# Performance work log

Measured on AMD Instinct MI355X. Metric: run time of the kernel, lower is better.

## Reference

```python
import jax, jax.numpy as jnp
import numpy as np
from jax import lax

B, N, C = 32, 2048, 256
S, NSAMP, RADIUS = 128, 16, 0.3
NH, NS, NC = 12, 10, 10
OUT_DIM = 5 + 2 * NH + 4 * NS + NC  # 79
EPS = 1e-5
MEAN_SIZES = np.array([[0.76584, 1.398258, 0.472728], [2.114256, 1.6203, 0.927272], [0.404671, 1.071108, 1.688889], [0.591958, 0.552978, 0.827272], [0.69519, 1.346299, 0.736364], [0.528526, 1.002642, 1.172878], [0.500618, 0.632163, 0.683424], [0.923508, 1.867419, 0.845495], [0.791118, 1.279516, 0.718182], [0.699104, 0.454178, 0.75625]], dtype=np.float32)


def _bn(x, g, be, m, v):
    # eval-mode batchnorm over trailing channel dim
    return (x - m) * (g / jnp.sqrt(v + EPS)) + be


def _fps(xyz, npoint):
    # farthest point sampling, sequential over npoint via scan, vectorized over batch
    Bb, Nn, _ = xyz.shape
    def step(carry, _):
        mind, last = carry  # [B,N], [B]
        lp = jnp.take_along_axis(xyz, last[:, None, None], axis=1)  # [B,1,3]
        d = jnp.sum((xyz - lp) ** 2, axis=-1)
        mind = jnp.minimum(mind, d)
        nxt = jnp.argmax(mind, axis=-1).astype(jnp.int32)
        return (mind, nxt), last
    init = (jnp.full((Bb, Nn), 1e10, xyz.dtype), jnp.zeros((Bb,), jnp.int32))
    _, inds = lax.scan(step, init, None, length=npoint)
    return jnp.transpose(inds)  # [B, npoint]


def _ball_query(xyz, new_xyz, radius, nsample):
    # first-nsample points within radius of each center (pad with first hit)
    Nn = xyz.shape[1]
    d2 = jnp.sum((new_xyz[:, :, None, :] - xyz[:, None, :, :]) ** 2, axis=-1)  # [B,S,N]
    cand = jnp.where(d2 < radius * radius, jnp.arange(Nn, dtype=jnp.int32)[None, None, :], Nn)
    idx = jnp.sort(cand, axis=-1)[..., :nsample]
    first = idx[..., :1]  # center itself is always within radius (d=0)
    return jnp.where(idx == Nn, first, idx)


def _forward(xyz, features, w0, bb0, g0, be0, m0, v0, w1, bb1, g1, be1, m1, v1, w2, bb2, g2, be2, m2, v2, c1w, c1b, g3, be3, m3, v3, c2w, c2b, g4, be4, m4, v4, c3w, c3b):
    fps_idx = _fps(xyz, S)  # [B,S]
    new_xyz = jnp.take_along_axis(xyz, fps_idx[..., None], axis=1)  # [B,S,3]
    idx = _ball_query(xyz, new_xyz, RADIUS, NSAMP)  # [B,S,ns]
    bidx = jnp.arange(xyz.shape[0])[:, None, None]
    g_xyz = (xyz[bidx, idx] - new_xyz[:, :, None, :]) / RADIUS  # normalize_xyz
    g_feat = jnp.transpose(features, (0, 2, 1))[bidx, idx]  # [B,S,ns,C]
    x = jnp.concatenate([g_xyz, g_feat], axis=-1)  # [B,S,ns,C+3]
    for w, bb, g, be, m, v in ((w0, bb0, g0, be0, m0, v0), (w1, bb1, g1, be1, m1, v1), (w2, bb2, g2, be2, m2, v2)):
        x = jax.nn.relu(_bn(x @ w + bb, g, be, m, v))
    x = jnp.max(x, axis=2)  # [B,S,128] pooled features
    net = jax.nn.relu(_bn(x @ c1w + c1b, g3, be3, m3, v3))
    net = jax.nn.relu(_bn(net @ c2w + c2b, g4, be4, m4, v4))
    net = net @ c3w + c3b  # [B,S,79] == torch net.transpose(2,1)
    obj = net[..., 0:2]
    ctr = new_xyz + net[..., 2:5]
    hs = net[..., 5:5 + NH]
    hrn = net[..., 5 + NH:5 + 2 * NH]
    hr = hrn * jnp.float32(np.pi / NH)
    ss = net[..., 5 + 2 * NH:5 + 2 * NH + NS]
    srn = net[..., 5 + 2 * NH + NS:5 + 2 * NH + 4 * NS].reshape(net.shape[0], S, NS, 3)
    sr = srn * jnp.asarray(MEAN_SIZES)[None, None]
    sem = net[..., 5 + 2 * NH + 4 * NS:]
    return jnp.concatenate([new_xyz, obj, ctr, hs, hrn, hr, ss, srn.reshape(net.shape[0], S, NS * 3), sr.reshape(net.shape[0], S, NS * 3), sem], axis=-1)  # [B,S,124]


def setup_inputs() -> dict:
    key = jax.random.key(0)
    ks = jax.random.split(key, 40)
    def w(k, shp):
        return jax.random.normal(k, shp, jnp.float32) * 0.05
    d = {"xyz": jax.random.normal(ks[0], (B, N, 3), jnp.float32), "features": jax.random.normal(ks[1], (B, C, N), jnp.float32)}
    i = 2
    for li, (cin, cout) in enumerate(((C + 3, 128), (128, 128), (128, 128))):
        d[f"w{li}"] = w(ks[i], (cin, cout)); d[f"bb{li}"] = w(ks[i + 1], (cout,))
        d[f"g{li}"] = 1.0 + w(ks[i + 2], (cout,)); d[f"be{li}"] = w(ks[i + 3], (cout,))
        d[f"m{li}"] = w(ks[i + 4], (cout,)); d[f"v{li}"] = jnp.ones((cout,), jnp.float32)
        i += 5
    d["c1w"] = w(ks[i], (128, 128)); d["c1b"] = w(ks[i + 1], (128,))
    d["g3"] = 1.0 + w(ks[i + 2], (128,)); d["be3"] = w(ks[i + 3], (128,)); d["m3"] = w(ks[i + 4], (128,)); d["v3"] = jnp.ones((128,), jnp.float32)
    d["c2w"] = w(ks[i + 5], (128, 128)); d["c2b"] = w(ks[i + 6], (128,))
    d["g4"] = 1.0 + w(ks[i + 7], (128,)); d["be4"] = w(ks[i + 8], (128,)); d["m4"] = w(ks[i + 9], (128,)); d["v4"] = jnp.ones((128,), jnp.float32)
    d["c3w"] = w(ks[i + 10], (128, OUT_DIM)); d["c3b"] = w(ks[i + 11], (OUT_DIM,))
    return d


def reference(xyz, features, w0, bb0, g0, be0, m0, v0, w1, bb1, g1, be1, m1, v1, w2, bb2, g2, be2, m2, v2, c1w, c1b, g3, be3, m3, v3, c2w, c2b, g4, be4, m4, v4, c3w, c3b):
    return _forward(xyz, features, w0, bb0, g0, be0, m0, v0, w1, bb1, g1, be1, m1, v1, w2, bb2, g2, be2, m2, v2, c1w, c1b, g3, be3, m3, v3, c2w, c2b, g4, be4, m4, v4, c3w, c3b)
```

## Files before the change

kernel.cpp:

```cpp
#include <hip/hip_runtime.h>
#include <hip/hip_bf16.h>
#include <math.h>

#define Bn 32
#define Nn 2048
#define Cc 256
#define Sn 128
#define KK 16
#define H 128
#define OUTC 79
#define ODIM 124
#define KP1 288

typedef __attribute__((ext_vector_type(8))) short short8;
typedef __attribute__((ext_vector_type(4))) float f32x4;
typedef unsigned long long ull;

__device__ __constant__ float MEANF[30] = {
    0.76584f, 1.398258f, 0.472728f,
    2.114256f, 1.6203f, 0.927272f,
    0.404671f, 1.071108f, 1.688889f,
    0.591958f, 0.552978f, 0.827272f,
    0.69519f, 1.346299f, 0.736364f,
    0.528526f, 1.002642f, 1.172878f,
    0.500618f, 0.632163f, 0.683424f,
    0.923508f, 1.867419f, 0.845495f,
    0.791118f, 1.279516f, 0.718182f,
    0.699104f, 0.454178f, 0.75625f};

__device__ __forceinline__ unsigned short f2bf(float f) {
    __hip_bfloat16 h = __float2bfloat16(f);
    return *reinterpret_cast<unsigned short*>(&h);
}

__device__ __forceinline__ ull umax64(ull a, ull b) { return a > b ? a : b; }

#define DPPMAX(CTRL, RM)                                                        \
    {                                                                           \
        const int nhi = __builtin_amdgcn_update_dpp(0, hi, CTRL, RM, 0xf, false); \
        const int nlo = __builtin_amdgcn_update_dpp(0, lo, CTRL, RM, 0xf, false); \
        const ull nk = ((ull)(unsigned)nhi << 32) | (unsigned)nlo;              \
        const ull ck = ((ull)(unsigned)hi << 32) | (unsigned)lo;                \
        if (nk > ck) { hi = nhi; lo = nlo; }                                    \
    }

struct SmemFPS {
    float xs[Nn * 3];
    ull red[2][4];
    float nx[Sn * 3];
};
struct SmemT {
    float tile[64][33];
};
__global__ __launch_bounds__(256) void fps_transpose_kernel(const float* __restrict__ xyz,
                                                            const float* __restrict__ features,
                                                            float* __restrict__ new_xyz,
                                                            unsigned short* __restrict__ fT) {
    __shared__ __align__(16) char smem_raw[sizeof(SmemT) > sizeof(SmemFPS) ? sizeof(SmemT)
                                                                           : sizeof(SmemFPS)];
    const int bid = blockIdx.x;
    if (bid >= Bn) {
        SmemT* sm = (SmemT*)smem_raw;
        const int tb = bid - Bn;
        const int b = tb >> 8;
        const int rem = tb & 255;
        const int n0 = (rem & 63) * 32;
        const int c0 = (rem >> 6) * 64;
        const int tx = threadIdx.x & 31;
        const int ty = threadIdx.x >> 5;
        for (int i = ty; i < 64; i += 8)
            sm->tile[i][tx] = features[((size_t)b * Cc + (c0 + i)) * Nn + n0 + tx];
        __syncthreads();
        for (int n = ty; n < 32; n += 8) {
            const float lo = sm->tile[tx * 2 + 0][n];
            const float hi = sm->tile[tx * 2 + 1][n];
            const unsigned int v = (unsigned int)f2bf(lo) | ((unsigned int)f2bf(hi) << 16);
            *reinterpret_cast<unsigned int*>(&fT[((size_t)b * Nn + (n0 + n)) * Cc + c0 + tx * 2]) = v;
        }
        return;
    }
    {
#pragma clang fp contract(off)
        SmemFPS* sm = (SmemFPS*)smem_raw;
        float* xs = sm->xs;
        const int b = bid;
        const int t = threadIdx.x;
        const int lane = t & 63;
        const int wv = t >> 6;

        {
            float4* xs4 = (float4*)xs;
            const float4* src = (const float4*)(xyz + (size_t)b * Nn * 3);
            for (int i = t; i < Nn * 3 / 4; i += 256) xs4[i] = src[i];
        }
        __syncthreads();

        const int base = wv * 512 + lane;
        float px[8], py[8], pz[8], mind[8];
        int klo[8];
#pragma unroll
        for (int j = 0; j < 8; j++) {
            const int p = base + j * 64;
            px[j] = xs[p * 3 + 0];
            py[j] = xs[p * 3 + 1];
            pz[j] = xs[p * 3 + 2];
            mind[j] = 1e10f;
            klo[j] = 2047 - p;
        }
        float lx = xs[0], ly = xs[1], lz = xs[2];

        for (int it = 0; it < Sn; ++it) {
            if (t == 0) {
                sm->nx[it * 3 + 0] = lx;
                sm->nx[it * 3 + 1] = ly;
                sm->nx[it * 3 + 2] = lz;
            }
            ull kk[8];
#pragma unroll
            for (int j = 0; j < 8; j++) {
                const float dx = px[j] - lx;
                const float dy = py[j] - ly;
                const float dz = pz[j] - lz;
                const float dx2 = dx * dx;
                const float dy2 = dy * dy;
                const float dz2 = dz * dz;
                const float s01 = dx2 + dy2;
                const float d = s01 + dz2;
                const float m = fminf(mind[j], d);
                mind[j] = m;
                kk[j] = ((ull)__float_as_uint(m) << 32) | (unsigned int)klo[j];
            }
            ull k0 = umax64(kk[0], kk[1]);
            ull k1 = umax64(kk[2], kk[3]);
            ull k2 = umax64(kk[4], kk[5]);
            ull k3 = umax64(kk[6], kk[7]);
            k0 = umax64(k0, k1);
            k2 = umax64(k2, k3);
            const ull bk0 = umax64(k0, k2);

            int hi = (int)(bk0 >> 32);
            int lo = (int)(bk0 & 0xffffffffull);
            DPPMAX(0x111, 0xf)
            DPPMAX(0x112, 0xf)
            DPPMAX(0x114, 0xf)
            DPPMAX(0x118, 0xf)
            DPPMAX(0x142, 0xa)
            DPPMAX(0x143, 0xc)

            if (lane == 63)
                sm->red[it & 1][wv] = ((ull)(unsigned)hi << 32) | (unsigned)lo;
            __syncthreads();
            ull r0 = sm->red[it & 1][0];
            ull r1 = sm->red[it & 1][1];
            ull r2 = sm->red[it & 1][2];
            ull r3 = sm->red[it & 1][3];
            const ull bk = umax64(umax64(r0, r1), umax64(r2, r3));
            const int last = 2047 - (int)(bk & 0xffffffffull);
            lx = xs[last * 3 + 0];
            ly = xs[last * 3 + 1];
            lz = xs[last * 3 + 2];
        }
        __syncthreads();
        for (int i = t; i < Sn * 3; i += 256)
            new_xyz[(size_t)b * Sn * 3 + i] = sm->nx[i];
    }
}

__device__ __forceinline__ float w0val(const float* __restrict__ w0, int n, int k) {
    if (k < 256) return w0[(3 + k) * H + n];
    if (k < 259) return w0[(k - 256) * H + n];
    return 0.0f;
}

__global__ __launch_bounds__(256) void prep_kernel(
    const float* __restrict__ w0, const float* __restrict__ bb0,
    const float* __restrict__ g0, const float* __restrict__ be0,
    const float* __restrict__ m0, const float* __restrict__ v0,
    const float* __restrict__ w1, const float* __restrict__ bb1,
    const float* __restrict__ g1, const float* __restrict__ be1,
    const float* __restrict__ m1, const float* __restrict__ v1,
    const float* __restrict__ w2, const float* __restrict__ bb2,
    const float* __restrict__ g2, const float* __restrict__ be2,
    const float* __restrict__ m2, const float* __restrict__ v2,
    const float* __restrict__ c1w, const float* __restrict__ c1b,
    const float* __restrict__ g3, const float* __restrict__ be3,
    const float* __restrict__ m3, const float* __restrict__ v3,
    const float* __restrict__ c2w, const float* __restrict__ c2b,
    const float* __restrict__ g4, const float* __restrict__ be4,
    const float* __restrict__ m4, const float* __restrict__ v4,
    const float* __restrict__ c3w, const float* __restrict__ c3b,
    unsigned short* __restrict__ Wf0, unsigned short* __restrict__ Wf1,
    unsigned short* __restrict__ Wf2, unsigned short* __restrict__ Wfc1,
    unsigned short* __restrict__ Wfc2, unsigned short* __restrict__ Wfc3,
    float* __restrict__ scbi, float* __restrict__ scbiH) {
    const int idx = blockIdx.x * 256 + threadIdx.x;

    if (idx < 4608) {
        const int kc = idx / 512;
        const int rem = idx & 511;
        const int nt = rem >> 6;
        const int lane = rem & 63;
        const int n = nt * 16 + (lane & 15);
        const int kb = kc * 32 + (lane >> 4) * 8;
        union { unsigned short u[8]; uint4 q; } P;
#pragma unroll
        for (int j = 0; j < 8; j++) P.u[j] = f2bf(w0val(w0, n, kb + j));
        ((uint4*)Wf0)[idx] = P.q;
    }
    if (idx < 2048) {
        const int kc = idx >> 9;
        const int rem = idx & 511;
        const int nt = rem >> 6;
        const int lane = rem & 63;
        const int n = nt * 16 + (lane & 15);
        const int kb = kc * 32 + (lane >> 4) * 8;
        union { unsigned short u[8]; uint4 q; } P1, P2, P3, P4;
#pragma unroll
        for (int j = 0; j < 8; j++) {
            const int k = kb + j;
            P1.u[j] = f2bf(w1[k * H + n]);
            P2.u[j] = f2bf(w2[k * H + n]);
            P3.u[j] = f2bf(c1w[k * H + n]);
            P4.u[j] = f2bf(c2w[k * H + n]);
        }
        ((uint4*)Wf1)[idx] = P1.q;
        ((uint4*)Wf2)[idx] = P2.q;
        ((uint4*)Wfc1)[idx] = P3.q;
        ((uint4*)Wfc2)[idx] = P4.q;
    }
    if (idx < 1280) {
        const int kc = idx / 320;
        const int rem = idx % 320;
        const int nt = rem / 64;
        const int lane = rem % 64;
        const int n = nt * 16 + (lane & 15);
        const int kb = kc * 32 + (lane >> 4) * 8;
        union { unsigned short u[8]; uint4 q; } P;
#pragma unroll
        for (int j = 0; j < 8; j++)
            P.u[j] = (n < OUTC) ? f2bf(c3w[(kb + j) * OUTC + n]) : (unsigned short)0;
        ((uint4*)Wfc3)[idx] = P.q;
    }
    if (idx < 128) {
        const float sc1 = g0[idx] / sqrtf(v0[idx] + 1e-5f);
        scbi[0 * 128 + idx] = sc1;
        scbi[1 * 128 + idx] = (bb0[idx] - m0[idx]) * sc1 + be0[idx];
        const float sc2 = g1[idx] / sqrtf(v1[idx] + 1e-5f);
        scbi[2 * 128 + idx] = sc2;
        scbi[3 * 128 + idx] = (bb1[idx] - m1[idx]) * sc2 + be1[idx];
        const float sc3 = g2[idx] / sqrtf(v2[idx] + 1e-5f);
        scbi[4 * 128 + idx] = sc3;
        scbi[5 * 128 + idx] = (bb2[idx] - m2[idx]) * sc3 + be2[idx];
        const float sA = g3[idx] / sqrtf(v3[idx] + 1e-5f);
        scbiH[0 * 128 + idx] = sA;
        scbiH[1 * 128 + idx] = (c1b[idx] - m3[idx]) * sA + be3[idx];
        const float sB = g4[idx] / sqrtf(v4[idx] + 1e-5f);
        scbiH[2 * 128 + idx] = sB;
        scbiH[3 * 128 + idx] = (c2b[idx] - m4[idx]) * sB + be4[idx];
    }
    if (idx < 80) scbiH[512 + idx] = (idx < OUTC) ? c3b[idx] : 0.0f;
}

#define YSTR 136
__global__ __launch_bounds__(256) void groupmlp_mfma_kernel(
    const float* __restrict__ xyz, const unsigned short* __restrict__ featT,
    const float* __restrict__ new_xyz,
    const unsigned short* __restrict__ Wf0, const unsigned short* __restrict__ Wf1,
    const unsigned short* __restrict__ Wf2, const float* __restrict__ scbi,
    unsigned short* __restrict__ pooledb) {
    const int wv = threadIdx.x >> 6;
    const int lane = threadIdx.x & 63;
    const int bs = blockIdx.x * 4 + wv;
    const int b = bs >> 7;
    const int mrow = lane & 15;
    const int quad = lane >> 4;

    __shared__ unsigned short ylds_all[4][16 * YSTR];
    __shared__ int sbuf[4][16];
    unsigned short* ylds = &ylds_all[wv][0];

    const float cx = new_xyz[bs * 3 + 0];
    const float cy = new_xyz[bs * 3 + 1];
    const float cz = new_xyz[bs * 3 + 2];
    int basec = 0;
    {
#pragma clang fp contract(off)
        for (int c0 = 0; c0 < Nn && basec < KK; c0 += 64) {
            const int p = c0 + lane;
            const float dx = xyz[((size_t)b * Nn + p) * 3 + 0] - cx;
            const float dy = xyz[((size_t)b * Nn + p) * 3 + 1] - cy;
            const float dz = xyz[((size_t)b * Nn + p) * 3 + 2] - cz;
            const float dx2 = dx * dx;
            const float dy2 = dy * dy;
            const float dz2 = dz * dz;
            const float s01 = dx2 + dy2;
            const float d2 = s01 + dz2;
            const bool q = d2 < 0.09f;
            const ull mask = __ballot(q);
            const int prefix = __popcll(mask & ((1ull << lane) - 1ull));
            const int slot = basec + prefix;
            if (q && slot < KK) sbuf[wv][slot] = p;
            basec += __popcll(mask);
        }
    }
    const int cnt = basec < KK ? basec : KK;
    const int p = sbuf[wv][mrow < cnt ? mrow : 0];

    const short8* arow = reinterpret_cast<const short8*>(featT + ((size_t)(b * Nn + p)) * Cc);

    short8 a1x = {0, 0, 0, 0, 0, 0, 0, 0};
    {
        const float fx = xyz[((size_t)(b * Nn + p)) * 3 + 0];
        const float fy = xyz[((size_t)(b * Nn + p)) * 3 + 1];
        const float fz = xyz[((size_t)(b * Nn + p)) * 3 + 2];
        if (quad == 0) {
            a1x.s0 = (short)f2bf((fx - cx) / 0.3f);
            a1x.s1 = (short)f2bf((fy - cy) / 0.3f);
            a1x.s2 = (short)f2bf((fz - cz) / 0.3f);
        }
    }

    const short8* wf0 = reinterpret_cast<const short8*>(Wf0);
    const short8* wf1 = reinterpret_cast<const short8*>(Wf1);
    const short8* wf2 = reinterpret_cast<const short8*>(Wf2);
    const short8* yv = reinterpret_cast<const short8*>(ylds);

    f32x4 acc[8] = {};

    {
        short8 acur = arow[quad];
        short8 anxt;
        short8 bcur[8], bnxt[8];
#pragma unroll
        for (int nt = 0; nt < 8; nt++)
            bcur[nt] = wf0[nt * 64 + lane];
        for (int kc = 0; kc < 9; kc++) {
            if (kc < 8) {
                if (kc < 7) anxt = arow[(kc + 1) * 4 + quad];
                else anxt = a1x;
#pragma unroll
                for (int nt = 0; nt < 8; nt++)
                    bnxt[nt] = wf0[((kc + 1) * 8 + nt) * 64 + lane];
            }
#pragma unroll
            for (int nt = 0; nt < 8; nt++)
                acc[nt] = __builtin_amdgcn_mfma_f32_16x16x32_bf16(acur, bcur[nt], acc[nt], 0, 0, 0);
            acur = anxt;
#pragma unroll
            for (int nt = 0; nt < 8; nt++) bcur[nt] = bnxt[nt];
        }
    }
#pragma unroll
    for (int nt = 0; nt < 8; nt++) {
        const int n = nt * 16 + mrow;
        const float sc = scbi[0 * 128 + n];
        const float bi = scbi[1 * 128 + n];
#pragma unroll
        for (int r = 0; r < 4; r++) {
            const float z = fmaxf(acc[nt][r] * sc + bi, 0.0f);
            ylds[(quad * 4 + r) * YSTR + n] = f2bf(z);
        }
    }

#pragma unroll
    for (int nt = 0; nt < 8; nt++) acc[nt] = (f32x4){0.f, 0.f, 0.f, 0.f};
    {
        short8 acur = yv[mrow * (YSTR / 8) + quad];
        short8 anxt;
        short8 bcur[8], bnxt[8];
#pragma unroll
        for (int nt = 0; nt < 8; nt++)
            bcur[nt] = wf1[nt * 64 + lane];
        for (int kc = 0; kc < 4; kc++) {
            if (kc < 3) {
                anxt = yv[mrow * (YSTR / 8) + (kc + 1) * 4 + quad];
#pragma unroll
                for (int nt = 0; nt < 8; nt++)
                    bnxt[nt] = wf1[((kc + 1) * 8 + nt) * 64 + lane];
            }
#pragma unroll
            for (int nt = 0; nt < 8; nt++)
                acc[nt] = __builtin_amdgcn_mfma_f32_16x16x32_bf16(acur, bcur[nt], acc[nt], 0, 0, 0);
            acur = anxt;
#pragma unroll
            for (int nt = 0; nt < 8; nt++) bcur[nt] = bnxt[nt];
        }
    }
#pragma unroll
    for (int nt = 0; nt < 8; nt++) {
        const int n = nt * 16 + mrow;
        const float sc = scbi[2 * 128 + n];
        const float bi = scbi[3 * 128 + n];
#pragma unroll
        for (int r = 0; r < 4; r++) {
            const float z = fmaxf(acc[nt][r] * sc + bi, 0.0f);
            ylds[(quad * 4 + r) * YSTR + n] = f2bf(z);
        }
    }

#pragma unroll
    for (int nt = 0; nt < 8; nt++) acc[nt] = (f32x4){0.f, 0.f, 0.f, 0.f};
    {
        short8 acur = yv[mrow * (YSTR / 8) + quad];
        short8 anxt;
        short8 bcur[8], bnxt[8];
#pragma unroll
        for (int nt = 0; nt < 8; nt++)
            bcur[nt] = wf2[nt * 64 + lane];
        for (int kc = 0; kc < 4; kc++) {
            if (kc < 3) {
                anxt = yv[mrow * (YSTR / 8) + (kc + 1) * 4 + quad];
#pragma unroll
                for (int nt = 0; nt < 8; nt++)
                    bnxt[nt] = wf2[((kc + 1) * 8 + nt) * 64 + lane];
            }
#pragma unroll
            for (int nt = 0; nt < 8; nt++)
                acc[nt] = __builtin_amdgcn_mfma_f32_16x16x32_bf16(acur, bcur[nt], acc[nt], 0, 0, 0);
            acur = anxt;
#pragma unroll
            for (int nt = 0; nt < 8; nt++) bcur[nt] = bnxt[nt];
        }
    }
#pragma unroll
    for (int nt = 0; nt < 8; nt++) {
        const int n = nt * 16 + mrow;
        const float sc = scbi[4 * 128 + n];
        const float bi = scbi[5 * 128 + n];
        float vmax = 0.0f;
#pragma unroll
        for (int r = 0; r < 4; r++)
            vmax = fmaxf(vmax, acc[nt][r] * sc + bi);
        vmax = fmaxf(vmax, __shfl_xor(vmax, 16));
        vmax = fmaxf(vmax, __shfl_xor(vmax, 32));
        if (quad == 0) pooledb[(size_t)bs * H + n] = f2bf(vmax);
    }
}

__global__ __launch_bounds__(64) void head_mfma_kernel(
    const unsigned short* __restrict__ pooledb, const float* __restrict__ new_xyz,
    const unsigned short* __restrict__ Wfc1, const unsigned short* __restrict__ Wfc2,
    const unsigned short* __restrict__ Wfc3, const float* __restrict__ scbiH,
    float* __restrict__ out) {
    const int lane = threadIdx.x;
    const int row0 = blockIdx.x * 16;
    const int mrow = lane & 15;
    const int quad = lane >> 4;

    __shared__ unsigned short ylds[16 * YSTR];
    __shared__ float flds[16 * 84];

    const short8* ar = reinterpret_cast<const short8*>(pooledb + (size_t)(row0 + mrow) * H);
    const short8* w1h = reinterpret_cast<const short8*>(Wfc1);
    const short8* w2h = reinterpret_cast<const short8*>(Wfc2);
    const short8* w3h = reinterpret_cast<const short8*>(Wfc3);
    const short8* yv = reinterpret_cast<const short8*>(ylds);

    f32x4 acc[8] = {};
#pragma unroll
    for (int kc = 0; kc < 4; kc++) {
        const short8 a = ar[kc * 4 + quad];
#pragma unroll
        for (int nt = 0; nt < 8; nt++) {
            const short8 bf = w1h[(kc * 8 + nt) * 64 + lane];
            acc[nt] = __builtin_amdgcn_mfma_f32_16x16x32_bf16(a, bf, acc[nt], 0, 0, 0);
        }
    }
#pragma unroll
    for (int nt = 0; nt < 8; nt++) {
        const int n = nt * 16 + mrow;
        const float sc = scbiH[0 * 128 + n];
        const float bi = scbiH[1 * 128 + n];
#pragma unroll
        for (int r = 0; r < 4; r++) {
            const float z = fmaxf(acc[nt][r] * sc + bi, 0.0f);
            ylds[(quad * 4 + r) * YSTR + n] = f2bf(z);
        }
    }

#pragma unroll
    for (int nt = 0; nt < 8; nt++) acc[nt] = (f32x4){0.f, 0.f, 0.f, 0.f};
#pragma unroll
    for (int kc = 0; kc < 4; kc++) {
        const short8 a = yv[mrow * (YSTR / 8) + kc * 4 + quad];
#pragma unroll
        for (int nt = 0; nt < 8; nt++) {
            const short8 bf = w2h[(kc * 8 + nt) * 64 + lane];
            acc[nt] = __builtin_amdgcn_mfma_f32_16x16x32_bf16(a, bf, acc[nt], 0, 0, 0);
        }
    }
#pragma unroll
    for (int nt = 0; nt < 8; nt++) {
        const int n = nt * 16 + mrow;
        const float sc = scbiH[2 * 128 + n];
        const float bi = scbiH[3 * 128 + n];
#pragma unroll
        for (int r = 0; r < 4; r++) {
            const float z = fmaxf(acc[nt][r] * sc + bi, 0.0f);
            ylds[(quad * 4 + r) * YSTR + n] = f2bf(z);
        }
    }

    f32x4 acc3[5] = {};
#pragma unroll
    for (int kc = 0; kc < 4; kc++) {
        const short8 a = yv[mrow * (YSTR / 8) + kc * 4 + quad];
#pragma unroll
        for (int nt = 0; nt < 5; nt++) {
            const short8 bf = w3h[(kc * 5 + nt) * 64 + lane];
            acc3[nt] = __builtin_amdgcn_mfma_f32_16x16x32_bf16(a, bf, acc3[nt], 0, 0, 0);
        }
    }
#pragma unroll
    for (int nt = 0; nt < 5; nt++) {
        const int n = nt * 16 + mrow;
        const float bi = scbiH[512 + n];
#pragma unroll
        for (int r = 0; r < 4; r++)
            flds[(quad * 4 + r) * 84 + n] = acc3[nt][r] + bi;
    }

    for (int m = 0; m < 16; m++) {
        const int row = row0 + m;
        const float* net = &flds[m * 84];
        const float* nz = new_xyz + (size_t)row * 3;
#pragma unroll
        for (int jj = 0; jj < 2; jj++) {
            const int j = lane + jj * 64;
            if (j < ODIM) {
                float val;
                if (j < 3) val = nz[j];
                else if (j < 5) val = net[j - 3];
                else if (j < 8) val = nz[j - 5] + net[2 + (j - 5)];
                else if (j < 20) val = net[5 + (j - 8)];
                else if (j < 32) val = net[17 + (j - 20)];
                else if (j < 44) val = net[17 + (j - 32)] * (float)(3.14159265358979323846 / 12.0);
                else if (j < 54) val = net[29 + (j - 44)];
                else if (j < 84) val = net[39 + (j - 54)];
                else if (j < 114) val = net[39 + (j - 84)] * MEANF[j - 84];
                else val = net[69 + (j - 114)];
                out[(size_t)row * ODIM + j] = val;
            }
        }
    }
}

extern "C" void kernel_launch(void* const* d_in, const int* in_sizes, int n_in,
                              void* d_out, int out_size, void* d_ws, size_t ws_size,
                              hipStream_t stream) {
    (void)in_sizes; (void)n_in; (void)out_size; (void)ws_size;
    const float* xyz = (const float*)d_in[0];
    const float* features = (const float*)d_in[1];
    const float* w0 = (const float*)d_in[2];
    const float* bb0 = (const float*)d_in[3];
    const float* g0 = (const float*)d_in[4];
    const float* be0 = (const float*)d_in[5];
    const float* m0 = (const float*)d_in[6];
    const float* v0 = (const float*)d_in[7];
    const float* w1 = (const float*)d_in[8];
    const float* bb1 = (const float*)d_in[9];
    const float* g1 = (const float*)d_in[10];
    const float* be1 = (const float*)d_in[11];
    const float* m1 = (const float*)d_in[12];
    const float* v1 = (const float*)d_in[13];
    const float* w2 = (const float*)d_in[14];
    const float* bb2 = (const float*)d_in[15];
    const float* g2 = (const float*)d_in[16];
    const float* be2 = (const float*)d_in[17];
    const float* m2 = (const float*)d_in[18];
    const float* v2 = (const float*)d_in[19];
    const float* c1w = (const float*)d_in[20];
    const float* c1b = (const float*)d_in[21];
    const float* g3 = (const float*)d_in[22];
    const float* be3 = (const float*)d_in[23];
    const float* m3 = (const float*)d_in[24];
    const float* v3 = (const float*)d_in[25];
    const float* c2w = (const float*)d_in[26];
    const float* c2b = (const float*)d_in[27];
    const float* g4 = (const float*)d_in[28];
    const float* be4 = (const float*)d_in[29];
    const float* m4 = (const float*)d_in[30];
    const float* v4 = (const float*)d_in[31];
    const float* c3w = (const float*)d_in[32];
    const float* c3b = (const float*)d_in[33];
    float* out = (float*)d_out;

    char* ws = (char*)d_ws;
    float* nxyz = (float*)(ws + 0);
    float* scbi = (float*)(ws + 49152);
    float* scbiH = (float*)(ws + 52224);
    unsigned short* Wf0 = (unsigned short*)(ws + 54592);
    unsigned short* Wf1 = (unsigned short*)(ws + 128320);
    unsigned short* Wf2 = (unsigned short*)(ws + 161088);
    unsigned short* Wfc1 = (unsigned short*)(ws + 193856);
    unsigned short* Wfc2 = (unsigned short*)(ws + 226624);
    unsigned short* Wfc3 = (unsigned short*)(ws + 259392);
    unsigned short* pooledb = (unsigned short*)(ws + 279872);
    unsigned short* featT = (unsigned short*)(ws + 804160);

    hipLaunchKernelGGL(prep_kernel, dim3(18), dim3(256), 0, stream,
                       w0, bb0, g0, be0, m0, v0,
                       w1, bb1, g1, be1, m1, v1,
                       w2, bb2, g2, be2, m2, v2,
                       c1w, c1b, g3, be3, m3, v3,
                       c2w, c2b, g4, be4, m4, v4,
                       c3w, c3b,
                       Wf0, Wf1, Wf2, Wfc1, Wfc2, Wfc3, scbi, scbiH);
    hipLaunchKernelGGL(fps_transpose_kernel, dim3(Bn + Bn * 256), dim3(256), 0, stream,
                       xyz, features, nxyz, featT);
    hipLaunchKernelGGL(groupmlp_mfma_kernel, dim3(Bn * Sn / 4), dim3(256), 0, stream,
                       xyz, featT, nxyz, Wf0, Wf1, Wf2, scbi, pooledb);
    hipLaunchKernelGGL(head_mfma_kernel, dim3(Bn * Sn / 16), dim3(64), 0, stream,
                       pooledb, nxyz, Wfc1, Wfc2, Wfc3, scbiH, out);
}
```

Baseline: 279.9 us.

## Merge prep into front kernel and fuse group MLP with head MLP

Weight preparation now runs as extra blocks of the FPS/transpose kernel, which cuts the launch count from four to two. The grouped MLP and the head MLP are fused into one tail kernel. Each 256-thread block now handles 16 centers: pooled features stay in LDS as bf16, and the head GEMMs are split across four waves with block barriers between stages. This removes the pooled-feature round trip through global memory and two launch gaps, at the cost of fewer, larger tail blocks (256 instead of 1024 blocks) and extra synchronisation.

```diff
diff --git a/kernel.cpp b/kernel.cpp
--- a/kernel.cpp
+++ b/kernel.cpp
@@ -11,6 +11,7 @@
 #define OUTC 79
 #define ODIM 124
 #define KP1 288
+#define YSTR 136
 
 typedef __attribute__((ext_vector_type(8))) short short8;
 typedef __attribute__((ext_vector_type(4))) float f32x4;
@@ -35,13 +36,19 @@
 
 __device__ __forceinline__ ull umax64(ull a, ull b) { return a > b ? a : b; }
 
-#define DPPMAX(CTRL, RM)                                                        \
-    {                                                                           \
+__device__ __forceinline__ float w0val(const float* __restrict__ w0, int n, int k) {
+    if (k < 256) return w0[(3 + k) * H + n];
+    if (k < 259) return w0[(k - 256) * H + n];
+    return 0.0f;
+}
+
+#define DPPMAX(CTRL, RM)                                                          \
+    {                                                                             \
         const int nhi = __builtin_amdgcn_update_dpp(0, hi, CTRL, RM, 0xf, false); \
         const int nlo = __builtin_amdgcn_update_dpp(0, lo, CTRL, RM, 0xf, false); \
-        const ull nk = ((ull)(unsigned)nhi << 32) | (unsigned)nlo;              \
-        const ull ck = ((ull)(unsigned)hi << 32) | (unsigned)lo;                \
-        if (nk > ck) { hi = nhi; lo = nlo; }                                    \
+        const ull nk = ((ull)(unsigned)nhi << 32) | (unsigned)nlo;                \
+        const ull ck = ((ull)(unsigned)hi << 32) | (unsigned)lo;                  \
+        if (nk > ck) { hi = nhi; lo = nlo; }                                      \
     }
 
 struct SmemFPS {
@@ -52,127 +59,9 @@
 struct SmemT {
     float tile[64][33];
 };
-__global__ __launch_bounds__(256) void fps_transpose_kernel(const float* __restrict__ xyz,
-                                                            const float* __restrict__ features,
-                                                            float* __restrict__ new_xyz,
-                                                            unsigned short* __restrict__ fT) {
-    __shared__ __align__(16) char smem_raw[sizeof(SmemT) > sizeof(SmemFPS) ? sizeof(SmemT)
-                                                                           : sizeof(SmemFPS)];
-    const int bid = blockIdx.x;
-    if (bid >= Bn) {
-        SmemT* sm = (SmemT*)smem_raw;
-        const int tb = bid - Bn;
-        const int b = tb >> 8;
-        const int rem = tb & 255;
-        const int n0 = (rem & 63) * 32;
-        const int c0 = (rem >> 6) * 64;
-        const int tx = threadIdx.x & 31;
-        const int ty = threadIdx.x >> 5;
-        for (int i = ty; i < 64; i += 8)
-            sm->tile[i][tx] = features[((size_t)b * Cc + (c0 + i)) * Nn + n0 + tx];
-        __syncthreads();
-        for (int n = ty; n < 32; n += 8) {
-            const float lo = sm->tile[tx * 2 + 0][n];
-            const float hi = sm->tile[tx * 2 + 1][n];
-            const unsigned int v = (unsigned int)f2bf(lo) | ((unsigned int)f2bf(hi) << 16);
-            *reinterpret_cast<unsigned int*>(&fT[((size_t)b * Nn + (n0 + n)) * Cc + c0 + tx * 2]) = v;
-        }
-        return;
-    }
-    {
-#pragma clang fp contract(off)
-        SmemFPS* sm = (SmemFPS*)smem_raw;
-        float* xs = sm->xs;
-        const int b = bid;
-        const int t = threadIdx.x;
-        const int lane = t & 63;
-        const int wv = t >> 6;
-
-        {
-            float4* xs4 = (float4*)xs;
-            const float4* src = (const float4*)(xyz + (size_t)b * Nn * 3);
-            for (int i = t; i < Nn * 3 / 4; i += 256) xs4[i] = src[i];
-        }
-        __syncthreads();
-
-        const int base = wv * 512 + lane;
-        float px[8], py[8], pz[8], mind[8];
-        int klo[8];
-#pragma unroll
-        for (int j = 0; j < 8; j++) {
-            const int p = base + j * 64;
-            px[j] = xs[p * 3 + 0];
-            py[j] = xs[p * 3 + 1];
-            pz[j] = xs[p * 3 + 2];
-            mind[j] = 1e10f;
-            klo[j] = 2047 - p;
-        }
-        float lx = xs[0], ly = xs[1], lz = xs[2];
-
-        for (int it = 0; it < Sn; ++it) {
-            if (t == 0) {
-                sm->nx[it * 3 + 0] = lx;
-                sm->nx[it * 3 + 1] = ly;
-                sm->nx[it * 3 + 2] = lz;
-            }
-            ull kk[8];
-#pragma unroll
-            for (int j = 0; j < 8; j++) {
-                const float dx = px[j] - lx;
-                const float dy = py[j] - ly;
-                const float dz = pz[j] - lz;
-                const float dx2 = dx * dx;
-                const float dy2 = dy * dy;
-                const float dz2 = dz * dz;
-                const float s01 = dx2 + dy2;
-                const float d = s01 + dz2;
-                const float m = fminf(mind[j], d);
-                mind[j] = m;
-                kk[j] = ((ull)__float_as_uint(m) << 32) | (unsigned int)klo[j];
-            }
-            ull k0 = umax64(kk[0], kk[1]);
-            ull k1 = umax64(kk[2], kk[3]);
-            ull k2 = umax64(kk[4], kk[5]);
-            ull k3 = umax64(kk[6], kk[7]);
-            k0 = umax64(k0, k1);
-            k2 = umax64(k2, k3);
-            const ull bk0 = umax64(k0, k2);
-
-            int hi = (int)(bk0 >> 32);
-            int lo = (int)(bk0 & 0xffffffffull);
-            DPPMAX(0x111, 0xf)
-            DPPMAX(0x112, 0xf)
-            DPPMAX(0x114, 0xf)
-            DPPMAX(0x118, 0xf)
-            DPPMAX(0x142, 0xa)
-            DPPMAX(0x143, 0xc)
-
-            if (lane == 63)
-                sm->red[it & 1][wv] = ((ull)(unsigned)hi << 32) | (unsigned)lo;
-            __syncthreads();
-            ull r0 = sm->red[it & 1][0];
-            ull r1 = sm->red[it & 1][1];
-            ull r2 = sm->red[it & 1][2];
-            ull r3 = sm->red[it & 1][3];
-            const ull bk = umax64(umax64(r0, r1), umax64(r2, r3));
-            const int last = 2047 - (int)(bk & 0xffffffffull);
-            lx = xs[last * 3 + 0];
-            ly = xs[last * 3 + 1];
-            lz = xs[last * 3 + 2];
-        }
-        __syncthreads();
-        for (int i = t; i < Sn * 3; i += 256)
-            new_xyz[(size_t)b * Sn * 3 + i] = sm->nx[i];
-    }
-}
-
-__device__ __forceinline__ float w0val(const float* __restrict__ w0, int n, int k) {
-    if (k < 256) return w0[(3 + k) * H + n];
-    if (k < 259) return w0[(k - 256) * H + n];
-    return 0.0f;
-}
-
-__global__ __launch_bounds__(256) void prep_kernel(
+__global__ __launch_bounds__(256) void front_kernel(
+    const float* __restrict__ xyz, const float* __restrict__ features,
+    float* __restrict__ new_xyz, unsigned short* __restrict__ fT,
     const float* __restrict__ w0, const float* __restrict__ bb0,
     const float* __restrict__ g0, const float* __restrict__ be0,
     const float* __restrict__ m0, const float* __restrict__ v0,
@@ -193,334 +82,445 @@
     unsigned short* __restrict__ Wf2, unsigned short* __restrict__ Wfc1,
     unsigned short* __restrict__ Wfc2, unsigned short* __restrict__ Wfc3,
     float* __restrict__ scbi, float* __restrict__ scbiH) {
-    const int idx = blockIdx.x * 256 + threadIdx.x;
-
-    if (idx < 4608) {
-        const int kc = idx / 512;
-        const int rem = idx & 511;
-        const int nt = rem >> 6;
-        const int lane = rem & 63;
-        const int n = nt * 16 + (lane & 15);
-        const int kb = kc * 32 + (lane >> 4) * 8;
-        union { unsigned short u[8]; uint4 q; } P;
-#pragma unroll
-        for (int j = 0; j < 8; j++) P.u[j] = f2bf(w0val(w0, n, kb + j));
-        ((uint4*)Wf0)[idx] = P.q;
-    }
-    if (idx < 2048) {
-        const int kc = idx >> 9;
-        const int rem = idx & 511;
-        const int nt = rem >> 6;
-        const int lane = rem & 63;
-        const int n = nt * 16 + (lane & 15);
-        const int kb = kc * 32 + (lane >> 4) * 8;
-        union { unsigned short u[8]; uint4 q; } P1, P2, P3, P4;
+    __shared__ __align__(16) char smem_raw[sizeof(SmemT) > sizeof(SmemFPS) ? sizeof(SmemT)
+                                                                           : sizeof(SmemFPS)];
+    const int bid = blockIdx.x;
+    if (bid >= Bn + 8192) {
+        const int idx = (bid - (Bn + 8192)) * 256 + threadIdx.x;
+        if (idx < 4608) {
+            const int kc = idx / 512;
+            const int rem = idx & 511;
+            const int nt = rem >> 6;
+            const int ln = rem & 63;
+            const int n = nt * 16 + (ln & 15);
+            const int kb = kc * 32 + (ln >> 4) * 8;
+            union { unsigned short u[8]; uint4 q; } P;
+#pragma unroll
+            for (int j = 0; j < 8; j++) P.u[j] = f2bf(w0val(w0, n, kb + j));
+            ((uint4*)Wf0)[idx] = P.q;
+        }
+        if (idx < 2048) {
+            const int kc = idx >> 9;
+            const int rem = idx & 511;
+            const int nt = rem >> 6;
+            const int ln = rem & 63;
+            const int n = nt * 16 + (ln & 15);
+            const int kb = kc * 32 + (ln >> 4) * 8;
+            union { unsigned short u[8]; uint4 q; } P1, P2, P3, P4;
+#pragma unroll
+            for (int j = 0; j < 8; j++) {
+                const int k = kb + j;
+                P1.u[j] = f2bf(w1[k * H + n]);
+                P2.u[j] = f2bf(w2[k * H + n]);
+                P3.u[j] = f2bf(c1w[k * H + n]);
+                P4.u[j] = f2bf(c2w[k * H + n]);
+            }
+            ((uint4*)Wf1)[idx] = P1.q;
+            ((uint4*)Wf2)[idx] = P2.q;
+            ((uint4*)Wfc1)[idx] = P3.q;
+            ((uint4*)Wfc2)[idx] = P4.q;
+        }
+        if (idx < 1280) {
+            const int kc = idx / 320;
+            const int rem = idx % 320;
+            const int nt = rem / 64;
+            const int ln = rem % 64;
+            const int n = nt * 16 + (ln & 15);
+            const int kb = kc * 32 + (ln >> 4) * 8;
+            union { unsigned short u[8]; uint4 q; } P;
+#pragma unroll
+            for (int j = 0; j < 8; j++)
+                P.u[j] = (n < OUTC) ? f2bf(c3w[(kb + j) * OUTC + n]) : (unsigned short)0;
+            ((uint4*)Wfc3)[idx] = P.q;
+        }
+        if (idx < 128) {
+            const float sc1 = g0[idx] / sqrtf(v0[idx] + 1e-5f);
+            scbi[0 * 128 + idx] = sc1;
+            scbi[1 * 128 + idx] = (bb0[idx] - m0[idx]) * sc1 + be0[idx];
+            const float sc2 = g1[idx] / sqrtf(v1[idx] + 1e-5f);
+            scbi[2 * 128 + idx] = sc2;
+            scbi[3 * 128 + idx] = (bb1[idx] - m1[idx]) * sc2 + be1[idx];
+            const float sc3 = g2[idx] / sqrtf(v2[idx] + 1e-5f);
+            scbi[4 * 128 + idx] = sc3;
+            scbi[5 * 128 + idx] = (bb2[idx] - m2[idx]) * sc3 + be2[idx];
+            const float sA = g3[idx] / sqrtf(v3[idx] + 1e-5f);
+            scbiH[0 * 128 + idx] = sA;
+            scbiH[1 * 128 + idx] = (c1b[idx] - m3[idx]) * sA + be3[idx];
+            const float sB = g4[idx] / sqrtf(v4[idx] + 1e-5f);
+            scbiH[2 * 128 + idx] = sB;
+            scbiH[3 * 128 + idx] = (c2b[idx] - m4[idx]) * sB + be4[idx];
+        }
+        if (idx < 80) scbiH[512 + idx] = (idx < OUTC) ? c3b[idx] : 0.0f;
+        return;
+    }
+    if (bid >= Bn) {
+        SmemT* sm = (SmemT*)smem_raw;
+        const int tb = bid - Bn;
+        const int b = tb >> 8;
+        const int rem = tb & 255;
+        const int n0 = (rem & 63) * 32;
+        const int c0 = (rem >> 6) * 64;
+        const int tx = threadIdx.x & 31;
+        const int ty = threadIdx.x >> 5;
+        for (int i = ty; i < 64; i += 8)
+            sm->tile[i][tx] = features[((size_t)b * Cc + (c0 + i)) * Nn + n0 + tx];
+        __syncthreads();
+        for (int n = ty; n < 32; n += 8) {
+            const float lo2 = sm->tile[tx * 2 + 0][n];
+            const float hi2 = sm->tile[tx * 2 + 1][n];
+            const unsigned int v = (unsigned int)f2bf(lo2) | ((unsigned int)f2bf(hi2) << 16);
+            *reinterpret_cast<unsigned int*>(&fT[((size_t)b * Nn + (n0 + n)) * Cc + c0 + tx * 2]) = v;
+        }
+        return;
+    }
+    {
+#pragma clang fp contract(off)
+        SmemFPS* sm = (SmemFPS*)smem_raw;
+        float* xs = sm->xs;
+        const int b = bid;
+        const int t = threadIdx.x;
+        const int lane = t & 63;
+        const int wv = t >> 6;
+
+        {
+            float4* xs4 = (float4*)xs;
+            const float4* src = (const float4*)(xyz + (size_t)b * Nn * 3);
+            for (int i = t; i < Nn * 3 / 4; i += 256) xs4[i] = src[i];
+        }
+        __syncthreads();
+
+        const int base = wv * 512 + lane;
+        float px[8], py[8], pz[8], mind[8];
+        int klo[8];
 #pragma unroll
         for (int j = 0; j < 8; j++) {
-            const int k = kb + j;
-            P1.u[j] = f2bf(w1[k * H + n]);
-            P2.u[j] = f2bf(w2[k * H + n]);
-            P3.u[j] = f2bf(c1w[k * H + n]);
-            P4.u[j] = f2bf(c2w[k * H + n]);
-        }
-        ((uint4*)Wf1)[idx] = P1.q;
-        ((uint4*)Wf2)[idx] = P2.q;
-        ((uint4*)Wfc1)[idx] = P3.q;
-        ((uint4*)Wfc2)[idx] = P4.q;
-    }
-    if (idx < 1280) {
-        const int kc = idx / 320;
-        const int rem = idx % 320;
-        const int nt = rem / 64;
-        const int lane = rem % 64;
-        const int n = nt * 16 + (lane & 15);
-        const int kb = kc * 32 + (lane >> 4) * 8;
-        union { unsigned short u[8]; uint4 q; } P;
-#pragma unroll
-        for (int j = 0; j < 8; j++)
-            P.u[j] = (n < OUTC) ? f2bf(c3w[(kb + j) * OUTC + n]) : (unsigned short)0;
-        ((uint4*)Wfc3)[idx] = P.q;
-    }
-    if (idx < 128) {
-        const float sc1 = g0[idx] / sqrtf(v0[idx] + 1e-5f);
-        scbi[0 * 128 + idx] = sc1;
-        scbi[1 * 128 + idx] = (bb0[idx] - m0[idx]) * sc1 + be0[idx];
-        const float sc2 = g1[idx] / sqrtf(v1[idx] + 1e-5f);
-        scbi[2 * 128 + idx] = sc2;
-        scbi[3 * 128 + idx] = (bb1[idx] - m1[idx]) * sc2 + be1[idx];
-        const float sc3 = g2[idx] / sqrtf(v2[idx] + 1e-5f);
-        scbi[4 * 128 + idx] = sc3;
-        scbi[5 * 128 + idx] = (bb2[idx] - m2[idx]) * sc3 + be2[idx];
-        const float sA = g3[idx] / sqrtf(v3[idx] + 1e-5f);
-        scbiH[0 * 128 + idx] = sA;
-        scbiH[1 * 128 + idx] = (c1b[idx] - m3[idx]) * sA + be3[idx];
-        const float sB = g4[idx] / sqrtf(v4[idx] + 1e-5f);
-        scbiH[2 * 128 + idx] = sB;
-        scbiH[3 * 128 + idx] = (c2b[idx] - m4[idx]) * sB + be4[idx];
-    }
-    if (idx < 80) scbiH[512 + idx] = (idx < OUTC) ? c3b[idx] : 0.0f;
+            const int p = base + j * 64;
+            px[j] = xs[p * 3 + 0];
+            py[j] = xs[p * 3 + 1];
+            pz[j] = xs[p * 3 + 2];
+            mind[j] = 1e10f;
+            klo[j] = 2047 - p;
+        }
+        float lx = xs[0], ly = xs[1], lz = xs[2];
+
+        for (int it = 0; it < Sn; ++it) {
+            if (t == 0) {
+                sm->nx[it * 3 + 0] = lx;
+                sm->nx[it * 3 + 1] = ly;
+                sm->nx[it * 3 + 2] = lz;
+            }
+            ull kk[8];
+#pragma unroll
+            for (int j = 0; j < 8; j++) {
+                const float dx = px[j] - lx;
+                const float dy = py[j] - ly;
+                const float dz = pz[j] - lz;
+                const float dx2 = dx * dx;
+                const float dy2 = dy * dy;
+                const float dz2 = dz * dz;
+                const float s01 = dx2 + dy2;
+                const float d = s01 + dz2;
+                const float m = fminf(mind[j], d);
+                mind[j] = m;
+                kk[j] = ((ull)__float_as_uint(m) << 32) | (unsigned int)klo[j];
+            }
+            ull k0 = umax64(kk[0], kk[1]);
+            ull k1 = umax64(kk[2], kk[3]);
+            ull k2 = umax64(kk[4], kk[5]);
+            ull k3 = umax64(kk[6], kk[7]);
+            k0 = umax64(k0, k1);
+            k2 = umax64(k2, k3);
+            const ull bk0 = umax64(k0, k2);
+
+            int hi = (int)(bk0 >> 32);
+            int lo = (int)(bk0 & 0xffffffffull);
+            DPPMAX(0x111, 0xf)
+            DPPMAX(0x112, 0xf)
+            DPPMAX(0x114, 0xf)
+            DPPMAX(0x118, 0xf)
+            DPPMAX(0x142, 0xa)
+            DPPMAX(0x143, 0xc)
+
+            if (lane == 63)
+                sm->red[it & 1][wv] = ((ull)(unsigned)hi << 32) | (unsigned)lo;
+            __syncthreads();
+            ull r0 = sm->red[it & 1][0];
+            ull r1 = sm->red[it & 1][1];
+            ull r2 = sm->red[it & 1][2];
+            ull r3 = sm->red[it & 1][3];
+            const ull bk = umax64(umax64(r0, r1), umax64(r2, r3));
+            const int last = 2047 - (int)(bk & 0xffffffffull);
+            lx = xs[last * 3 + 0];
+            ly = xs[last * 3 + 1];
+            lz = xs[last * 3 + 2];
+        }
+        __syncthreads();
+        for (int i = t; i < Sn * 3; i += 256)
+            new_xyz[(size_t)b * Sn * 3 + i] = sm->nx[i];
+    }
 }
 
-#define YSTR 136
-__global__ __launch_bounds__(256) void groupmlp_mfma_kernel(
+__global__ __launch_bounds__(256) void tail_kernel(
     const float* __restrict__ xyz, const unsigned short* __restrict__ featT,
     const float* __restrict__ new_xyz,
     const unsigned short* __restrict__ Wf0, const unsigned short* __restrict__ Wf1,
     const unsigned short* __restrict__ Wf2, const float* __restrict__ scbi,
-    unsigned short* __restrict__ pooledb) {
+    const unsigned short* __restrict__ Wfc1, const unsigned short* __restrict__ Wfc2,
+    const unsigned short* __restrict__ Wfc3, const float* __restrict__ scbiH,
+    float* __restrict__ out) {
     const int wv = threadIdx.x >> 6;
     const int lane = threadIdx.x & 63;
-    const int bs = blockIdx.x * 4 + wv;
-    const int b = bs >> 7;
     const int mrow = lane & 15;
     const int quad = lane >> 4;
+    const int row0 = blockIdx.x * 16;
 
     __shared__ unsigned short ylds_all[4][16 * YSTR];
+    __shared__ unsigned short plds[16 * YSTR];
+    __shared__ float flds[16 * 84];
     __shared__ int sbuf[4][16];
     unsigned short* ylds = &ylds_all[wv][0];
-
-    const float cx = new_xyz[bs * 3 + 0];
-    const float cy = new_xyz[bs * 3 + 1];
-    const float cz = new_xyz[bs * 3 + 2];
-    int basec = 0;
-    {
-#pragma clang fp contract(off)
-        for (int c0 = 0; c0 < Nn && basec < KK; c0 += 64) {
-            const int p = c0 + lane;
-            const float dx = xyz[((size_t)b * Nn + p) * 3 + 0] - cx;
-            const float dy = xyz[((size_t)b * Nn + p) * 3 + 1] - cy;
-            const float dz = xyz[((size_t)b * Nn + p) * 3 + 2] - cz;
-            const float dx2 = dx * dx;
-            const float dy2 = dy * dy;
-            const float dz2 = dz * dz;
-            const float s01 = dx2 + dy2;
-            const float d2 = s01 + dz2;
-            const bool q = d2 < 0.09f;
-            const ull mask = __ballot(q);
-            const int prefix = __popcll(mask & ((1ull << lane) - 1ull));
-            const int slot = basec + prefix;
-            if (q && slot < KK) sbuf[wv][slot] = p;
-            basec += __popcll(mask);
-        }
-    }
-    const int cnt = basec < KK ? basec : KK;
-    const int p = sbuf[wv][mrow < cnt ? mrow : 0];
-
-    const short8* arow = reinterpret_cast<const short8*>(featT + ((size_t)(b * Nn + p)) * Cc);
-
-    short8 a1x = {0, 0, 0, 0, 0, 0, 0, 0};
-    {
-        const float fx = xyz[((size_t)(b * Nn + p)) * 3 + 0];
-        const float fy = xyz[((size_t)(b * Nn + p)) * 3 + 1];
-        const float fz = xyz[((size_t)(b * Nn + p)) * 3 + 2];
-        if (quad == 0) {
-            a1x.s0 = (short)f2bf((fx - cx) / 0.3f);
-            a1x.s1 = (short)f2bf((fy - cy) / 0.3f);
-            a1x.s2 = (short)f2bf((fz - cz) / 0.3f);
-        }
-    }
 
     const short8* wf0 = reinterpret_cast<const short8*>(Wf0);
     const short8* wf1 = reinterpret_cast<const short8*>(Wf1);
     const short8* wf2 = reinterpret_cast<const short8*>(Wf2);
     const short8* yv = reinterpret_cast<const short8*>(ylds);
 
-    f32x4 acc[8] = {};
-
-    {
-        short8 acur = arow[quad];
-        short8 anxt;
-        short8 bcur[8], bnxt[8];
-#pragma unroll
-        for (int nt = 0; nt < 8; nt++)
-            bcur[nt] = wf0[nt * 64 + lane];
-        for (int kc = 0; kc < 9; kc++) {
-            if (kc < 8) {
-                if (kc < 7) anxt = arow[(kc + 1) * 4 + quad];
-                else anxt = a1x;
+    for (int u = 0; u < 4; u++) {
+        const int bs = row0 + wv * 4 + u;
+        const int b = bs >> 7;
+
+        const float cx = new_xyz[bs * 3 + 0];
+        const float cy = new_xyz[bs * 3 + 1];
+        const float cz = new_xyz[bs * 3 + 2];
+        int basec = 0;
+        {
+#pragma clang fp contract(off)
+            for (int c0 = 0; c0 < Nn && basec < KK; c0 += 64) {
+                const int p = c0 + lane;
+                const float dx = xyz[((size_t)b * Nn + p) * 3 + 0] - cx;
+                const float dy = xyz[((size_t)b * Nn + p) * 3 + 1] - cy;
+                const float dz = xyz[((size_t)b * Nn + p) * 3 + 2] - cz;
+                const float dx2 = dx * dx;
+                const float dy2 = dy * dy;
+                const float dz2 = dz * dz;
+                const float s01 = dx2 + dy2;
+                const float d2 = s01 + dz2;
+                const bool q = d2 < 0.09f;
+                const ull mask = __ballot(q);
+                const int prefix = __popcll(mask & ((1ull << lane) - 1ull));
+                const int slot = basec + prefix;
+                if (q && slot < KK) sbuf[wv][slot] = p;
+                basec += __popcll(mask);
+            }
+        }
+        const int cnt = basec < KK ? basec : KK;
+        const int p = sbuf[wv][mrow < cnt ? mrow : 0];
+
+        const short8* arow = reinterpret_cast<const short8*>(featT + ((size_t)(b * Nn + p)) * Cc);
+
+        short8 a1x = {0, 0, 0, 0, 0, 0, 0, 0};
+        {
+            const float fx = xyz[((size_t)(b * Nn + p)) * 3 + 0];
+            const float fy = xyz[((size_t)(b * Nn + p)) * 3 + 1];
+            const float fz = xyz[((size_t)(b * Nn + p)) * 3 + 2];
+            if (quad == 0) {
+                a1x.s0 = (short)f2bf((fx - cx) / 0.3f);
+                a1x.s1 = (short)f2bf((fy - cy) / 0.3f);
+                a1x.s2 = (short)f2bf((fz - cz) / 0.3f);
+            }
+        }
+
+        f32x4 acc[8] = {};
+        {
+            short8 acur = arow[quad];
+            short8 anxt;
+            short8 bcur[8], bnxt[8];
+#pragma unroll
+            for (int nt = 0; nt < 8; nt++) bcur[nt] = wf0[nt * 64 + lane];
+            for (int kc = 0; kc < 9; kc++) {
+                if (kc < 8) {
+                    if (kc < 7) anxt = arow[(kc + 1) * 4 + quad];
+                    else anxt = a1x;
+#pragma unroll
+                    for (int nt = 0; nt < 8; nt++)
+                        bnxt[nt] = wf0[((kc + 1) * 8 + nt) * 64 + lane];
+                }
 #pragma unroll
                 for (int nt = 0; nt < 8; nt++)
-                    bnxt[nt] = wf0[((kc + 1) * 8 + nt) * 64 + lane];
-            }
-#pragma unroll
-            for (int nt = 0; nt < 8; nt++)
-                acc[nt] = __builtin_amdgcn_mfma_f32_16x16x32_bf16(acur, bcur[nt], acc[nt], 0, 0, 0);
-            acur = anxt;
-#pragma unroll
-            for (int nt = 0; nt < 8; nt++) bcur[nt] = bnxt[nt];
-        }
-    }
-#pragma unroll
-    for (int nt = 0; nt < 8; nt++) {
-        const int n = nt * 16 + mrow;
-        const float sc = scbi[0 * 128 + n];
-        const float bi = scbi[1 * 128 + n];
-#pragma unroll
-        for (int r = 0; r < 4; r++) {
-            const float z = fmaxf(acc[nt][r] * sc + bi, 0.0f);
-            ylds[(quad * 4 + r) * YSTR + n] = f2bf(z);
-        }
-    }
-
-#pragma unroll
-    for (int nt = 0; nt < 8; nt++) acc[nt] = (f32x4){0.f, 0.f, 0.f, 0.f};
-    {
-        short8 acur = yv[mrow * (YSTR / 8) + quad];
-        short8 anxt;
-        short8 bcur[8], bnxt[8];
-#pragma unroll
-        for (int nt = 0; nt < 8; nt++)
-            bcur[nt] = wf1[nt * 64 + lane];
-        for (int kc = 0; kc < 4; kc++) {
-            if (kc < 3) {
-                anxt = yv[mrow * (YSTR / 8) + (kc + 1) * 4 + quad];
+                    acc[nt] = __builtin_amdgcn_mfma_f32_16x16x32_bf16(acur, bcur[nt], acc[nt], 0, 0, 0);
+                acur = anxt;
+#pragma unroll
+                for (int nt = 0; nt < 8; nt++) bcur[nt] = bnxt[nt];
+            }
+        }
+#pragma unroll
+        for (int nt = 0; nt < 8; nt++) {
+            const int n = nt * 16 + mrow;
+            const float sc = scbi[0 * 128 + n];
+            const float bi = scbi[1 * 128 + n];
+#pragma unroll
+            for (int r = 0; r < 4; r++) {
+                const float z = fmaxf(acc[nt][r] * sc + bi, 0.0f);
+                ylds[(quad * 4 + r) * YSTR + n] = f2bf(z);
+            }
+        }
+
+#pragma unroll
+        for (int nt = 0; nt < 8; nt++) acc[nt] = (f32x4){0.f, 0.f, 0.f, 0.f};
+        {
+            short8 acur = yv[mrow * (YSTR / 8) + quad];
+            short8 anxt;
+            short8 bcur[8], bnxt[8];
+#pragma unroll
+            for (int nt = 0; nt < 8; nt++) bcur[nt] = wf1[nt * 64 + lane];
+            for (int kc = 0; kc < 4; kc++) {
+                if (kc < 3) {
+                    anxt = yv[mrow * (YSTR / 8) + (kc + 1) * 4 + quad];
+#pragma unroll
+                    for (int nt = 0; nt < 8; nt++)
+                        bnxt[nt] = wf1[((kc + 1) * 8 + nt) * 64 + lane];
+                }
 #pragma unroll
                 for (int nt = 0; nt < 8; nt++)
-                    bnxt[nt] = wf1[((kc + 1) * 8 + nt) * 64 + lane];
-            }
-#pragma unroll
-            for (int nt = 0; nt < 8; nt++)
-                acc[nt] = __builtin_amdgcn_mfma_f32_16x16x32_bf16(acur, bcur[nt], acc[nt], 0, 0, 0);
-            acur = anxt;
-#pragma unroll
-            for (int nt = 0; nt < 8; nt++) bcur[nt] = bnxt[nt];
-        }
-    }
-#pragma unroll
-    for (int nt = 0; nt < 8; nt++) {
-        const int n = nt * 16 + mrow;
-        const float sc = scbi[2 * 128 + n];
-        const float bi = scbi[3 * 128 + n];
-#pragma unroll
-        for (int r = 0; r < 4; r++) {
-            const float z = fmaxf(acc[nt][r] * sc + bi, 0.0f);
-            ylds[(quad * 4 + r) * YSTR + n] = f2bf(z);
-        }
-    }
-
-#pragma unroll
-    for (int nt = 0; nt < 8; nt++) acc[nt] = (f32x4){0.f, 0.f, 0.f, 0.f};
-    {
-        short8 acur = yv[mrow * (YSTR / 8) + quad];
-        short8 anxt;
-        short8 bcur[8], bnxt[8];
-#pragma unroll
-        for (int nt = 0; nt < 8; nt++)
-            bcur[nt] = wf2[nt * 64 + lane];
-        for (int kc = 0; kc < 4; kc++) {
-            if (kc < 3) {
-                anxt = yv[mrow * (YSTR / 8) + (kc + 1) * 4 + quad];
+                    acc[nt] = __builtin_amdgcn_mfma_f32_16x16x32_bf16(acur, bcur[nt], acc[nt], 0, 0, 0);
+                acur = anxt;
+#pragma unroll
+                for (int nt = 0; nt < 8; nt++) bcur[nt] = bnxt[nt];
+            }
+        }
+#pragma unroll
+        for (int nt = 0; nt < 8; nt++) {
+            const int n = nt * 16 + mrow;
+            const float sc = scbi[2 * 128 + n];
+            const float bi = scbi[3 * 128 + n];
+#pragma unroll
+            for (int r = 0; r < 4; r++) {
+                const float z = fmaxf(acc[nt][r] * sc + bi, 0.0f);
+                ylds[(quad * 4 + r) * YSTR + n] = f2bf(z);
+            }
+        }
+
+#pragma unroll
+        for (int nt = 0; nt < 8; nt++) acc[nt] = (f32x4){0.f, 0.f, 0.f, 0.f};
+        {
+            short8 acur = yv[mrow * (YSTR / 8) + quad];
+            short8 anxt;
+            short8 bcur[8], bnxt[8];
+#pragma unroll
+            for (int nt = 0; nt < 8; nt++) bcur[nt] = wf2[nt * 64 + lane];
+            for (int kc = 0; kc < 4; kc++) {
+                if (kc < 3) {
+                    anxt = yv[mrow * (YSTR / 8) + (kc + 1) * 4 + quad];
+#pragma unroll
+                    for (int nt = 0; nt < 8; nt++)
+                        bnxt[nt] = wf2[((kc + 1) * 8 + nt) * 64 + lane];
+                }
 #pragma unroll
                 for (int nt = 0; nt < 8; nt++)
-                    bnxt[nt] = wf2[((kc + 1) * 8 + nt) * 64 + lane];
-            }
-#pragma unroll
-            for (int nt = 0; nt < 8; nt++)
-                acc[nt] = __builtin_amdgcn_mfma_f32_16x16x32_bf16(acur, bcur[nt], acc[nt], 0, 0, 0);
-            acur = anxt;
-#pragma unroll
-            for (int nt = 0; nt < 8; nt++) bcur[nt] = bnxt[nt];
-        }
-    }
-#pragma unroll
-    for (int nt = 0; nt < 8; nt++) {
-        const int n = nt * 16 + mrow;
-        const float sc = scbi[4 * 128 + n];
-        const float bi = scbi[5 * 128 + n];
-        float vmax = 0.0f;
-#pragma unroll
-        for (int r = 0; r < 4; r++)
-            vmax = fmaxf(vmax, acc[nt][r] * sc + bi);
-        vmax = fmaxf(vmax, __shfl_xor(vmax, 16));
-        vmax = fmaxf(vmax, __shfl_xor(vmax, 32));
-        if (quad == 0) pooledb[(size_t)bs * H + n] = f2bf(vmax);
-    }
-}
-
-__global__ __launch_bounds__(64) void head_mfma_kernel(
-    const unsigned short* __restrict__ pooledb, const float* __restrict__ new_xyz,
-    const unsigned short* __restrict__ Wfc1, const unsigned short* __restrict__ Wfc2,
-    const unsigned short* __restrict__ Wfc3, const float* __restrict__ scbiH,
-    float* __restrict__ out) {
-    const int lane = threadIdx.x;
-    const int row0 = blockIdx.x * 16;
-    const int mrow = lane & 15;
-    const int quad = lane >> 4;
-
-    __shared__ unsigned short ylds[16 * YSTR];
-    __shared__ float flds[16 * 84];
-
-    const short8* ar = reinterpret_cast<const short8*>(pooledb + (size_t)(row0 + mrow) * H);
+                    acc[nt] = __builtin_amdgcn_mfma_f32_16x16x32_bf16(acur, bcur[nt], acc[nt], 0, 0, 0);
+                acur = anxt;
+#pragma unroll
+                for (int nt = 0; nt < 8; nt++) bcur[nt] = bnxt[nt];
+            }
+        }
+#pragma unroll
+        for (int nt = 0; nt < 8; nt++) {
+            const int n = nt * 16 + mrow;
+            const float sc = scbi[4 * 128 + n];
+            const float bi = scbi[5 * 128 + n];
+            float vmax = 0.0f;
+#pragma unroll
+            for (int r = 0; r < 4; r++)
+                vmax = fmaxf(vmax, acc[nt][r] * sc + bi);
+            vmax = fmaxf(vmax, __shfl_xor(vmax, 16));
+            vmax = fmaxf(vmax, __shfl_xor(vmax, 32));
+            if (quad == 0) plds[(wv * 4 + u) * YSTR + n] = f2bf(vmax);
+        }
+    }
+    __syncthreads();
+
+    unsigned short* yh = &ylds_all[0][0];
+    const short8* yhv = reinterpret_cast<const short8*>(yh);
+    const short8* pl = reinterpret_cast<const short8*>(plds);
     const short8* w1h = reinterpret_cast<const short8*>(Wfc1);
     const short8* w2h = reinterpret_cast<const short8*>(Wfc2);
     const short8* w3h = reinterpret_cast<const short8*>(Wfc3);
-    const short8* yv = reinterpret_cast<const short8*>(ylds);
-
-    f32x4 acc[8] = {};
-#pragma unroll
-    for (int kc = 0; kc < 4; kc++) {
-        const short8 a = ar[kc * 4 + quad];
-#pragma unroll
-        for (int nt = 0; nt < 8; nt++) {
-            const short8 bf = w1h[(kc * 8 + nt) * 64 + lane];
-            acc[nt] = __builtin_amdgcn_mfma_f32_16x16x32_bf16(a, bf, acc[nt], 0, 0, 0);
-        }
-    }
-#pragma unroll
-    for (int nt = 0; nt < 8; nt++) {
-        const int n = nt * 16 + mrow;
-        const float sc = scbiH[0 * 128 + n];
-        const float bi = scbiH[1 * 128 + n];
-#pragma unroll
-        for (int r = 0; r < 4; r++) {
-            const float z = fmaxf(acc[nt][r] * sc + bi, 0.0f);
-            ylds[(quad * 4 + r) * YSTR + n] = f2bf(z);
-        }
-    }
-
-#pragma unroll
-    for (int nt = 0; nt < 8; nt++) acc[nt] = (f32x4){0.f, 0.f, 0.f, 0.f};
-#pragma unroll
-    for (int kc = 0; kc < 4; kc++) {
-        const short8 a = yv[mrow * (YSTR / 8) + kc * 4 + quad];
-#pragma unroll
-        for (int nt = 0; nt < 8; nt++) {
-            const short8 bf = w2h[(kc * 8 + nt) * 64 + lane];
-            acc[nt] = __builtin_amdgcn_mfma_f32_16x16x32_bf16(a, bf, acc[nt], 0, 0, 0);
-        }
-    }
-#pragma unroll
-    for (int nt = 0; nt < 8; nt++) {
-        const int n = nt * 16 + mrow;
-        const float sc = scbiH[2 * 128 + n];
-        const float bi = scbiH[3 * 128 + n];
-#pragma unroll
-        for (int r = 0; r < 4; r++) {
-            const float z = fmaxf(acc[nt][r] * sc + bi, 0.0f);
-            ylds[(quad * 4 + r) * YSTR + n] = f2bf(z);
-        }
-    }
-
-    f32x4 acc3[5] = {};
-#pragma unroll
-    for (int kc = 0; kc < 4; kc++) {
-        const short8 a = yv[mrow * (YSTR / 8) + kc * 4 + quad];
-#pragma unroll
-        for (int nt = 0; nt < 5; nt++) {
-            const short8 bf = w3h[(kc * 5 + nt) * 64 + lane];
-            acc3[nt] = __builtin_amdgcn_mfma_f32_16x16x32_bf16(a, bf, acc3[nt], 0, 0, 0);
-        }
-    }
-#pragma unroll
-    for (int nt = 0; nt < 5; nt++) {
-        const int n = nt * 16 + mrow;
-        const float bi = scbiH[512 + n];
-#pragma unroll
-        for (int r = 0; r < 4; r++)
-            flds[(quad * 4 + r) * 84 + n] = acc3[nt][r] + bi;
-    }
-
-    for (int m = 0; m < 16; m++) {
+
+    {
+        f32x4 acc[2] = {};
+#pragma unroll
+        for (int kc = 0; kc < 4; kc++) {
+            const short8 a = pl[mrow * (YSTR / 8) + kc * 4 + quad];
+#pragma unroll
+            for (int i = 0; i < 2; i++) {
+                const int nt = wv * 2 + i;
+                const short8 bf = w1h[(kc * 8 + nt) * 64 + lane];
+                acc[i] = __builtin_amdgcn_mfma_f32_16x16x32_bf16(a, bf, acc[i], 0, 0, 0);
+            }
+        }
+#pragma unroll
+        for (int i = 0; i < 2; i++) {
+            const int nt = wv * 2 + i;
+            const int n = nt * 16 + mrow;
+            const float sc = scbiH[0 * 128 + n];
+            const float bi = scbiH[1 * 128 + n];
+#pragma unroll
+            for (int r = 0; r < 4; r++) {
+                const float z = fmaxf(acc[i][r] * sc + bi, 0.0f);
+                yh[(quad * 4 + r) * YSTR + n] = f2bf(z);
+            }
+        }
+    }
+    __syncthreads();
+
+    {
+        f32x4 acc[2] = {};
+#pragma unroll
+        for (int kc = 0; kc < 4; kc++) {
+            const short8 a = yhv[mrow * (YSTR / 8) + kc * 4 + quad];
+#pragma unroll
+            for (int i = 0; i < 2; i++) {
+                const int nt = wv * 2 + i;
+                const short8 bf = w2h[(kc * 8 + nt) * 64 + lane];
+                acc[i] = __builtin_amdgcn_mfma_f32_16x16x32_bf16(a, bf, acc[i], 0, 0, 0);
+            }
+        }
+        __syncthreads();
+#pragma unroll
+        for (int i = 0; i < 2; i++) {
+            const int nt = wv * 2 + i;
+            const int n = nt * 16 + mrow;
+            const float sc = scbiH[2 * 128 + n];
+            const float bi = scbiH[3 * 128 + n];
+#pragma unroll
+            for (int r = 0; r < 4; r++) {
+                const float z = fmaxf(acc[i][r] * sc + bi, 0.0f);
+                yh[(quad * 4 + r) * YSTR + n] = f2bf(z);
+            }
+        }
+    }
+    __syncthreads();
+
+    {
+        for (int nt = wv; nt < 5; nt += 4) {
+            f32x4 acc3 = {};
+#pragma unroll
+            for (int kc = 0; kc < 4; kc++) {
+                const short8 a = yhv[mrow * (YSTR / 8) + kc * 4 + quad];
+                const short8 bf = w3h[(kc * 5 + nt) * 64 + lane];
+                acc3 = __builtin_amdgcn_mfma_f32_16x16x32_bf16(a, bf, acc3, 0, 0, 0);
+            }
+            const int n = nt * 16 + mrow;
+            const float bi = scbiH[512 + n];
+#pragma unroll
+            for (int r = 0; r < 4; r++)
+                flds[(quad * 4 + r) * 84 + n] = acc3[r] + bi;
+        }
+    }
+    __syncthreads();
+
+    for (int i = 0; i < 4; i++) {
+        const int m = wv * 4 + i;
         const int row = row0 + m;
         const float* net = &flds[m * 84];
         const float* nz = new_xyz + (size_t)row * 3;
@@ -595,10 +595,10 @@
     unsigned short* Wfc1 = (unsigned short*)(ws + 193856);
     unsigned short* Wfc2 = (unsigned short*)(ws + 226624);
     unsigned short* Wfc3 = (unsigned short*)(ws + 259392);
-    unsigned short* pooledb = (unsigned short*)(ws + 279872);
-    unsigned short* featT = (unsigned short*)(ws + 804160);
-
-    hipLaunchKernelGGL(prep_kernel, dim3(18), dim3(256), 0, stream,
+    unsigned short* featT = (unsigned short*)(ws + 279872);
+
+    hipLaunchKernelGGL(front_kernel, dim3(Bn + 8192 + 18), dim3(256), 0, stream,
+                       xyz, features, nxyz, featT,
                        w0, bb0, g0, be0, m0, v0,
                        w1, bb1, g1, be1, m1, v1,
                        w2, bb2, g2, be2, m2, v2,
@@ -606,10 +606,7 @@
                        c2w, c2b, g4, be4, m4, v4,
                        c3w, c3b,
                        Wf0, Wf1, Wf2, Wfc1, Wfc2, Wfc3, scbi, scbiH);
-    hipLaunchKernelGGL(fps_transpose_kernel, dim3(Bn + Bn * 256), dim3(256), 0, stream,
-                       xyz, features, nxyz, featT);
-    hipLaunchKernelGGL(groupmlp_mfma_kernel, dim3(Bn * Sn / 4), dim3(256), 0, stream,
-                       xyz, featT, nxyz, Wf0, Wf1, Wf2, scbi, pooledb);
-    hipLaunchKernelGGL(head_mfma_kernel, dim3(Bn * Sn / 16), dim3(64), 0, stream,
-                       pooledb, nxyz, Wfc1, Wfc2, Wfc3, scbiH, out);
+    hipLaunchKernelGGL(tail_kernel, dim3(Bn * Sn / 16), dim3(256), 0, stream,
+                       xyz, featT, nxyz, Wf0, Wf1, Wf2, scbi,
+                       Wfc1, Wfc2, Wfc3, scbiH, out);
 }
```

Result: slower. 337.8 us (+20.7%).
